# Performance work log

Hardware: AMD Instinct MI355X
Metric: run time of the kernel (lower is better)

The kernel has to match this reference:

```python
import jax, jax.numpy as jnp
import numpy as np

B, N, D, NH, L, DFF = 2, 2048, 256, 8, 4, 1024
DH = D // NH
FACTOR = 0.5 / float(np.sqrt(DH))  # == 1/sqrt(4*DH), matches q/k feature dim 4*d_head
EPS = 1e-5


def _ln(x, g, b):
    m = x.mean(-1, keepdims=True)
    v = ((x - m) ** 2).mean(-1, keepdims=True)
    return (x - m) * jax.lax.rsqrt(v + EPS) * g + b


def setup_inputs() -> dict:
    key = jax.random.key(0)
    ks = jax.random.split(key, 16)
    s = 0.05
    r = lambda i, shape: jax.random.normal(ks[i], shape, dtype=jnp.float32)
    return {
        "H": r(0, (B, N, D)),
        "V": r(1, (B, N, 3, D)),
        "D_batch": r(2, (B, N, N)),
        "rbf_feat": r(3, (L, B, 1, N, N)),
        "H_mask": jnp.ones((B, N), dtype=bool),
        "ln1_g": jnp.ones((L, D)), "ln1_b": jnp.zeros((L, D)),
        "ln2_g": jnp.ones((L, D)), "ln2_b": jnp.zeros((L, D)),
        "Wq": r(4, (L, D, 4 * D)) * s, "bq": jnp.zeros((L, 4 * D)),
        "Wk": r(5, (L, D, 4 * D)) * s, "bk": jnp.zeros((L, 4 * D)),
        "Wv": r(6, (L, D, D)) * s, "bv": jnp.zeros((L, D)),
        "Wvv": r(7, (L, D, D)) * s,
        "Wo": r(8, (L, D, D)) * s, "bo": jnp.zeros((L, D)),
        "Wvo": r(9, (L, D, D)) * s,
        "Wlv": r(10, (L, D, 2 * D)) * s,
        "W1": r(11, (L, 2 * D, DFF)) * s, "b1": jnp.zeros((L, DFF)),
        "W2": r(12, (L, DFF, 2 * D)) * s, "b2": jnp.zeros((L, 2 * D)),
    }


def _stack_forward(H, V, D_batch, rbf_feat, H_mask, ln1_g, ln1_b, ln2_g, ln2_b,
                   Wq, bq, Wk, bk, Wv, bv, Wvv, Wo, bo, Wvo, Wlv, W1, b1, W2, b2):
    b, n = H.shape[:2]
    mask = H_mask[:, None, None, :]       # [B,1,1,N] masks key columns
    base_bias = D_batch[:, None]          # [B,1,N,N]

    def step(carry, xs):
        H, V = carry
        (rbf, g1, be1, g2, be2, wq, bq_, wk, bk_, wv, bv_, wvv,
         wo, bo_, wvo, wlv, w1, b1_, w2, b2_) = xs
        # --- self-attention sublayer (pre-LN on scalar stream only) ---
        Hn = _ln(H, g1, be1)
        Hq = (Hn @ wq + bq_).reshape(b, n, NH, 4 * DH)
        Hk = (Hn @ wk + bk_).reshape(b, n, NH, 4 * DH)
        Hv = (Hn @ wv + bv_).reshape(b, n, NH, DH)
        Vv = (V @ wvv).reshape(b, n, 3, NH, DH)
        Vv = jnp.swapaxes(Vv, 2, 3).reshape(b, n, NH, 3 * DH)
        V_attn = jnp.concatenate([Hv, Vv], axis=-1)        # [B,N,H,4*DH]
        bias = jnp.where(mask, rbf + base_bias, -jnp.inf)  # [B,1,N,N]
        scores = jnp.einsum('bnhd,bmhd->bhnm', Hq, Hk) * FACTOR + bias
        attn = jax.nn.softmax(scores, axis=-1)
        res = jnp.einsum('bhnm,bmhd->bnhd', attn, V_attn)  # [B,N,H,4*DH]
        H_res = res[..., :DH].reshape(b, n, D)
        V_res = jnp.swapaxes(res[..., DH:].reshape(b, n, NH, 3, DH), 2, 3).reshape(b, n, 3, D)
        H = H + (H_res @ wo + bo_)
        V = V + V_res @ wvo
        # --- GVP FFN sublayer (pre-LN on scalar stream only) ---
        Hn = _ln(H, g2, be2)
        Vp = V @ wlv                                       # [B,N,3,2D]
        V1, V2 = Vp[..., :D], Vp[..., D:]
        scaler = jnp.concatenate([Hn, jnp.linalg.norm(V1, axis=-2)], axis=-1)
        sc = jax.nn.silu(scaler @ w1 + b1_) @ w2 + b2_
        H = H + sc[..., :D]
        V = V + sc[..., D:][..., None, :] * V2             # vector_act='none'
        return (H, V), None

    xs = (rbf_feat, ln1_g, ln1_b, ln2_g, ln2_b, Wq, bq, Wk, bk, Wv, bv, Wvv,
          Wo, bo, Wvo, Wlv, W1, b1, W2, b2)
    (H, V), _ = jax.lax.scan(step, (H, V), xs)
    return H, V


def reference(H, V, D_batch, rbf_feat, H_mask, ln1_g, ln1_b, ln2_g, ln2_b,
              Wq, bq, Wk, bk, Wv, bv, Wvv, Wo, bo, Wvo, Wlv, W1, b1, W2, b2):
    return _stack_forward(H, V, D_batch, rbf_feat, H_mask, ln1_g, ln1_b, ln2_g, ln2_b,
                          Wq, bq, Wk, bk, Wv, bv, Wvv, Wo, bo, Wvo, Wlv, W1, b1, W2, b2)
```

## Files before the change

### kernel.cpp

```cpp
#include <hip/hip_runtime.h>
#include <math.h>

static constexpr int B_  = 2;
static constexpr int N_  = 2048;
static constexpr int D_  = 256;
static constexpr int NH_ = 8;
static constexpr int L_  = 4;
static constexpr int DH_ = 32;
static constexpr int DQ_ = 128;
static constexpr float FACTOR_ = 0.08838834764831845f;
static constexpr float LOG2E_  = 1.4426950408889634f;
static constexpr float EPS_ = 1e-5f;

typedef short    short8   __attribute__((ext_vector_type(8)));
typedef unsigned short us4 __attribute__((ext_vector_type(4)));
typedef unsigned short us8 __attribute__((ext_vector_type(8)));
typedef float    f32x4    __attribute__((ext_vector_type(4)));
typedef unsigned short us;

__device__ __forceinline__ us f2b(float f) {
  unsigned u = __float_as_uint(f);
  unsigned r = u + 0x7FFF + ((u >> 16) & 1);
  return (us)(r >> 16);
}
__device__ __forceinline__ float b2f(us u) {
  return __uint_as_float(((unsigned)u) << 16);
}
__device__ __forceinline__ float e2(float x) {
  return __builtin_amdgcn_exp2f(x);
}
__device__ __forceinline__ void gl_lds16(const void* g, void* l) {
  __builtin_amdgcn_global_load_lds(
      (const __attribute__((address_space(1))) void*)g,
      (__attribute__((address_space(3))) void*)l, 16, 0, 0);
}

__global__ __launch_bounds__(256) void ln_kernel(const float* __restrict__ X,
    const float* __restrict__ g, const float* __restrict__ b,
    us* __restrict__ Y, float* __restrict__ Xcopy) {
  __shared__ float p1[4], p2[4];
  int row = blockIdx.x, tid = threadIdx.x;
  float x = X[(size_t)row * D_ + tid];
  if (Xcopy) Xcopy[(size_t)row * D_ + tid] = x;
  float a = x, c = x * x;
  #pragma unroll
  for (int o = 32; o > 0; o >>= 1) {
    a += __shfl_xor(a, o, 64);
    c += __shfl_xor(c, o, 64);
  }
  if ((tid & 63) == 0) { p1[tid >> 6] = a; p2[tid >> 6] = c; }
  __syncthreads();
  float s1 = (p1[0] + p1[1]) + (p1[2] + p1[3]);
  float s2 = (p2[0] + p2[1]) + (p2[2] + p2[3]);
  float mean = s1 * (1.0f / D_);
  float var  = s2 * (1.0f / D_) - mean * mean;
  float inv  = rsqrtf(var + EPS_);
  Y[(size_t)row * D_ + tid] = f2b((x - mean) * inv * g[tid] + b[tid]);
}

__global__ __launch_bounds__(256) void conv_copy(const float* __restrict__ X,
    float* __restrict__ Yf, us* __restrict__ Y) {
  size_t i = ((size_t)blockIdx.x * 256 + threadIdx.x) * 4;
  float4 v = *(const float4*)&X[i];
  *(float4*)&Yf[i] = v;
  us4 o = { f2b(v.x), f2b(v.y), f2b(v.z), f2b(v.w) };
  *(us4*)&Y[i] = o;
}

struct WConvDesc {
  const float* src[9];
  unsigned dst[9];
  int K[9];
  int N[9];
  int start[10];
  int lstride[9];
};
__global__ __launch_bounds__(256) void wconv_kernel(WConvDesc d, us* __restrict__ Wb) {
  __shared__ float T[64][65];
  int bid0 = blockIdx.x, tid = threadIdx.x;
  int lay = bid0 / 480;
  int bid = bid0 - lay * 480;
  int j = 0;
  #pragma unroll
  for (int q = 0; q < 8; q++) if (bid >= d.start[q + 1]) j = q + 1;
  int t = bid - d.start[j];
  int K = d.K[j], N = d.N[j];
  int tpr = N >> 6;
  int tk = t / tpr, tn = t - tk * tpr;
  const float* src = d.src[j] + (size_t)lay * d.lstride[j];
  us* dst = Wb + (size_t)lay * 1966080u + d.dst[j];
  #pragma unroll
  for (int i = 0; i < 4; i++) {
    int r = i * 16 + (tid >> 4), c = (tid & 15) * 4;
    *(float4*)&T[r][c] = *(const float4*)&src[(size_t)(tk * 64 + r) * N + tn * 64 + c];
  }
  __syncthreads();
  #pragma unroll
  for (int i = 0; i < 4; i++) {
    int n = i * 16 + (tid >> 4), k = (tid & 15) * 4;
    us4 o = { f2b(T[k][n]), f2b(T[k + 1][n]), f2b(T[k + 2][n]), f2b(T[k + 3][n]) };
    *(us4*)&dst[(size_t)(tn * 64 + n) * K + tk * 64 + k] = o;
  }
}

__global__ __launch_bounds__(256, 3) void gemm_qkv(const us* __restrict__ A,
    const us* __restrict__ Wt, const float* __restrict__ bias,
    const float* __restrict__ bias2, const float* __restrict__ bias3,
    us* __restrict__ Cb, const float* __restrict__ R,
    const float* __restrict__ Dq, us* __restrict__ BiasOut, float oscale,
    const us* __restrict__ Vbm, const us* __restrict__ WtVV,
    us* __restrict__ Vvb) {
  constexpr int BM = 128, BN = 64, K = 256, Nc = 2304;
  __shared__ us As[2][BM * 64];
  __shared__ us Bs[2][BN * 64];
  const int tid = threadIdx.x;

  if (blockIdx.y >= 54) {
    const size_t total = (size_t)B_ * N_ * N_;
    const int nb = (gridDim.y - 54) * gridDim.x;
    const int bidl = (blockIdx.y - 54) * gridDim.x + blockIdx.x;
    const size_t step = (size_t)nb * 256 * 8;
    for (size_t i = ((size_t)bidl * 256 + tid) * 8; i < total; i += step) {
      float4 r0 = *(const float4*)&R[i];
      float4 r1 = *(const float4*)&R[i + 4];
      float4 d0 = *(const float4*)&Dq[i];
      float4 d1 = *(const float4*)&Dq[i + 4];
      us8 o = { f2b((r0.x + d0.x) * LOG2E_), f2b((r0.y + d0.y) * LOG2E_),
                f2b((r0.z + d0.z) * LOG2E_), f2b((r0.w + d0.w) * LOG2E_),
                f2b((r1.x + d1.x) * LOG2E_), f2b((r1.y + d1.y) * LOG2E_),
                f2b((r1.z + d1.z) * LOG2E_), f2b((r1.w + d1.w) * LOG2E_) };
      *(us8*)&BiasOut[i] = o;
    }
    return;
  }

  const int w = tid >> 6, l = tid & 63;
  const int lx = l & 15, ly = l >> 4;
  const int wr = w >> 1, wc = w & 1;
  const int swz = (lx & 7) << 4;
  const size_t rowb = (size_t)K * 2;

  if (blockIdx.y >= 32) {
    const int q = (blockIdx.y - 32) * 36 + blockIdx.x;
    if (q >= 768) return;
    const int bn = q & 3, bm = q >> 2;
    const char* Ag = (const char*)Vbm + (size_t)(bm * 64) * K * 2;
    const char* Bg = (const char*)WtVV + (size_t)(bn * 64) * K * 2;

    #define GSTAGE2(buf, k0)                                                  \
      do {                                                                    \
        _Pragma("unroll")                                                     \
        for (int j = 0; j < 2; j++) {                                         \
          int o = j * 4096 + tid * 16;                                        \
          int r = o >> 7, cb = o & 127;                                       \
          int sc = cb ^ ((r & 7) << 4);                                       \
          gl_lds16(Ag + (size_t)r * rowb + (size_t)(k0) * 2 + sc,             \
                   &As[buf][(j * 4096 + w * 1024) >> 1]);                     \
          gl_lds16(Bg + (size_t)r * rowb + (size_t)(k0) * 2 + sc,             \
                   &Bs[buf][(j * 4096 + w * 1024) >> 1]);                     \
        }                                                                     \
      } while (0)

    f32x4 acc[2][2];
    #pragma unroll
    for (int i = 0; i < 2; i++)
      #pragma unroll
      for (int j = 0; j < 2; j++) acc[i][j] = (f32x4){0.f, 0.f, 0.f, 0.f};

    int cur = 0;
    GSTAGE2(0, 0);
    __syncthreads();
    for (int k0 = 0; k0 < K; k0 += 64) {
      if (k0 + 64 < K) GSTAGE2(cur ^ 1, k0 + 64);
      #pragma unroll
      for (int s = 0; s < 2; s++) {
        short8 af[2], bf[2];
        #pragma unroll
        for (int mt = 0; mt < 2; mt++)
          af[mt] = *(const short8*)
              &As[cur][(((wr * 32 + mt * 16 + lx) * 128) + ((s * 64 + ly * 16) ^ swz)) >> 1];
        #pragma unroll
        for (int nt = 0; nt < 2; nt++)
          bf[nt] = *(const short8*)
              &Bs[cur][(((wc * 32 + nt * 16 + lx) * 128) + ((s * 64 + ly * 16) ^ swz)) >> 1];
        __builtin_amdgcn_s_setprio(1);
        #pragma unroll
        for (int mt = 0; mt < 2; mt++)
          #pragma unroll
          for (int nt = 0; nt < 2; nt++)
            acc[mt][nt] = __builtin_amdgcn_mfma_f32_16x16x32_bf16(af[mt], bf[nt], acc[mt][nt], 0, 0, 0);
        __builtin_amdgcn_s_setprio(0);
      }
      __syncthreads();
      cur ^= 1;
    }
    #undef GSTAGE2

    #pragma unroll
    for (int nt = 0; nt < 2; nt++) {
      const int n = bn * 64 + wc * 32 + nt * 16 + lx;
      #pragma unroll
      for (int mt = 0; mt < 2; mt++) {
        #pragma unroll
        for (int r = 0; r < 4; r++) {
          const int m = bm * 64 + wr * 32 + mt * 16 + ly * 4 + r;
          Vvb[(size_t)m * 256 + n] = f2b(acc[mt][nt][r]);
        }
      }
    }
    return;
  }

  const int bn = blockIdx.x, bm = blockIdx.y;
  const char* Ag = (const char*)A + (size_t)(bm * BM) * K * 2;
  const char* Bg = (const char*)Wt + (size_t)(bn * BN) * K * 2;

  #define GSTAGE(buf, k0)                                                     \
    do {                                                                      \
      _Pragma("unroll")                                                       \
      for (int j = 0; j < 4; j++) {                                           \
        int o = j * 4096 + tid * 16;                                          \
        int r = o >> 7, cb = o & 127;                                         \
        int sc = cb ^ ((r & 7) << 4);                                         \
        gl_lds16(Ag + (size_t)r * rowb + (size_t)(k0) * 2 + sc,               \
                 &As[buf][(j * 4096 + w * 1024) >> 1]);                       \
      }                                                                       \
      _Pragma("unroll")                                                       \
      for (int j = 0; j < 2; j++) {                                           \
        int o = j * 4096 + tid * 16;                                          \
        int r = o >> 7, cb = o & 127;                                         \
        int sc = cb ^ ((r & 7) << 4);                                         \
        gl_lds16(Bg + (size_t)r * rowb + (size_t)(k0) * 2 + sc,               \
                 &Bs[buf][(j * 4096 + w * 1024) >> 1]);                       \
      }                                                                       \
    } while (0)

  f32x4 acc[4][2];
  #pragma unroll
  for (int i = 0; i < 4; i++)
    #pragma unroll
    for (int j = 0; j < 2; j++) acc[i][j] = (f32x4){0.f, 0.f, 0.f, 0.f};

  int cur = 0;
  GSTAGE(0, 0);
  __syncthreads();
  for (int k0 = 0; k0 < K; k0 += 64) {
    if (k0 + 64 < K) GSTAGE(cur ^ 1, k0 + 64);
    #pragma unroll
    for (int s = 0; s < 2; s++) {
      short8 af[4], bf[2];
      #pragma unroll
      for (int mt = 0; mt < 4; mt++)
        af[mt] = *(const short8*)
            &As[cur][(((wr * 64 + mt * 16 + lx) * 128) + ((s * 64 + ly * 16) ^ swz)) >> 1];
      #pragma unroll
      for (int nt = 0; nt < 2; nt++)
        bf[nt] = *(const short8*)
            &Bs[cur][(((wc * 32 + nt * 16 + lx) * 128) + ((s * 64 + ly * 16) ^ swz)) >> 1];
      __builtin_amdgcn_s_setprio(1);
      #pragma unroll
      for (int mt = 0; mt < 4; mt++)
        #pragma unroll
        for (int nt = 0; nt < 2; nt++)
          acc[mt][nt] = __builtin_amdgcn_mfma_f32_16x16x32_bf16(af[mt], bf[nt], acc[mt][nt], 0, 0, 0);
      __builtin_amdgcn_s_setprio(0);
    }
    __syncthreads();
    cur ^= 1;
  }
  #undef GSTAGE

  #pragma unroll
  for (int nt = 0; nt < 2; nt++) {
    const int n = bn * BN + wc * 32 + nt * 16 + lx;
    float bval, osc = oscale;
    if (n < 1024)      { bval = bias[n]; }
    else if (n < 2048) { bval = bias2[n - 1024]; osc = 1.0f; }
    else               { bval = bias3[n - 2048]; osc = 1.0f; }
    #pragma unroll
    for (int mt = 0; mt < 4; mt++) {
      #pragma unroll
      for (int r = 0; r < 4; r++) {
        const int m = bm * BM + wr * 64 + mt * 16 + ly * 4 + r;
        float v = acc[mt][nt][r] + bval;
        Cb[(size_t)m * Nc + n] = f2b(v * osc);
      }
    }
  }
}

template<int BM, int BN, int BIAS, int ACC, int SILU, int WF, int WB, int QKV, int MINW>
__global__ __launch_bounds__(256, MINW) void gemm_v2(const us* __restrict__ A,
    const us* __restrict__ Wt, const float* __restrict__ bias,
    const float* __restrict__ bias2, const float* __restrict__ bias3,
    float* __restrict__ Cf, us* __restrict__ Cb,
    int M, int K, int Nc, float oscale) {
  constexpr int NFM = BM / 32, NFN = BN / 32;
  constexpr int WSM = NFM * 16, WSN = NFN * 16;
  constexpr int NLA = BM / 32, NLB = BN / 32;
  __shared__ us As[2][BM * 64];
  __shared__ us Bs[2][BN * 64];
  const int tid = threadIdx.x;
  const int w = tid >> 6, l = tid & 63;
  const int lx = l & 15, ly = l >> 4;
  const int wr = w >> 1, wc = w & 1;
  const int bn = blockIdx.x, bm = blockIdx.y;
  const int swz = (lx & 7) << 4;
  const char* Ag = (const char*)A + (size_t)(bm * BM) * K * 2;
  const char* Bg = (const char*)Wt + (size_t)(bn * BN) * K * 2;
  const size_t rowb = (size_t)K * 2;

  #define GSTAGE(buf, k0)                                                     \
    do {                                                                      \
      _Pragma("unroll")                                                       \
      for (int j = 0; j < NLA; j++) {                                         \
        int o = j * 4096 + tid * 16;                                          \
        int r = o >> 7, cb = o & 127;                                         \
        int sc = cb ^ ((r & 7) << 4);                                         \
        gl_lds16(Ag + (size_t)r * rowb + (size_t)(k0) * 2 + sc,               \
                 &As[buf][(j * 4096 + w * 1024) >> 1]);                       \
      }                                                                       \
      _Pragma("unroll")                                                       \
      for (int j = 0; j < NLB; j++) {                                         \
        int o = j * 4096 + tid * 16;                                          \
        int r = o >> 7, cb = o & 127;                                         \
        int sc = cb ^ ((r & 7) << 4);                                         \
        gl_lds16(Bg + (size_t)r * rowb + (size_t)(k0) * 2 + sc,               \
                 &Bs[buf][(j * 4096 + w * 1024) >> 1]);                       \
      }                                                                       \
    } while (0)

  f32x4 acc[NFM][NFN];
  #pragma unroll
  for (int i = 0; i < NFM; i++)
    #pragma unroll
    for (int j = 0; j < NFN; j++) acc[i][j] = (f32x4){0.f, 0.f, 0.f, 0.f};

  int cur = 0;
  GSTAGE(0, 0);
  __syncthreads();
  for (int k0 = 0; k0 < K; k0 += 64) {
    if (k0 + 64 < K) GSTAGE(cur ^ 1, k0 + 64);
    #pragma unroll
    for (int s = 0; s < 2; s++) {
      short8 af[NFM], bf[NFN];
      #pragma unroll
      for (int mt = 0; mt < NFM; mt++)
        af[mt] = *(const short8*)
            &As[cur][(((wr * WSM + mt * 16 + lx) * 128) + ((s * 64 + ly * 16) ^ swz)) >> 1];
      #pragma unroll
      for (int nt = 0; nt < NFN; nt++)
        bf[nt] = *(const short8*)
            &Bs[cur][(((wc * WSN + nt * 16 + lx) * 128) + ((s * 64 + ly * 16) ^ swz)) >> 1];
      __builtin_amdgcn_s_setprio(1);
      #pragma unroll
      for (int mt = 0; mt < NFM; mt++)
        #pragma unroll
        for (int nt = 0; nt < NFN; nt++)
          acc[mt][nt] = __builtin_amdgcn_mfma_f32_16x16x32_bf16(af[mt], bf[nt], acc[mt][nt], 0, 0, 0);
      __builtin_amdgcn_s_setprio(0);
    }
    __syncthreads();
    cur ^= 1;
  }
  #undef GSTAGE

  #pragma unroll
  for (int nt = 0; nt < NFN; nt++) {
    const int n = bn * BN + wc * WSN + nt * 16 + lx;
    float bval = 0.f, osc = oscale;
    if (QKV) {
      if (n < 1024)      { bval = bias[n]; }
      else if (n < 2048) { bval = bias2[n - 1024]; osc = 1.0f; }
      else               { bval = bias3[n - 2048]; osc = 1.0f; }
    } else if (BIAS) {
      bval = bias[n];
    }
    #pragma unroll
    for (int mt = 0; mt < NFM; mt++) {
      #pragma unroll
      for (int r = 0; r < 4; r++) {
        const int m = bm * BM + wr * WSM + mt * 16 + ly * 4 + r;
        float v = acc[mt][nt][r] + bval;
        if (SILU) v = v / (1.f + __expf(-v));
        size_t idx = (size_t)m * Nc + n;
        if (ACC) v += Cf[idx];
        if (WF) Cf[idx] = v;
        if (WB) Cb[idx] = f2b(v * osc);
      }
    }
  }
}

__global__ __launch_bounds__(256, 3) void gemm_wo(const us* __restrict__ Hres,
    const us* __restrict__ Vres, const us* __restrict__ WtO,
    const us* __restrict__ WtVO, const float* __restrict__ bo,
    float* __restrict__ Hs, float* __restrict__ Vs, us* __restrict__ Vb) {
  constexpr int K = 256, Nc = 256;
  __shared__ us As[2][64 * 64];
  __shared__ us Bs[2][64 * 64];
  const int tid = threadIdx.x;
  const int w = tid >> 6, l = tid & 63;
  const int lx = l & 15, ly = l >> 4;
  const int wr = w >> 1, wc = w & 1;
  const int bn = blockIdx.x, bm = blockIdx.y;
  const bool isH = bm < 64;
  const int mb = isH ? bm : bm - 64;
  const int swz = (lx & 7) << 4;
  const char* Ag = (const char*)(isH ? Hres : Vres) + (size_t)(mb * 64) * K * 2;
  const char* Bg = (const char*)(isH ? WtO : WtVO) + (size_t)(bn * 64) * K * 2;
  const size_t rowb = (size_t)K * 2;

  #define GSTAGE(buf, k0)                                                     \
    do {                                                                      \
      _Pragma("unroll")                                                       \
      for (int j = 0; j < 2; j++) {                                           \
        int o = j * 4096 + tid * 16;                                          \
        int r = o >> 7, cb = o & 127;                                         \
        int sc = cb ^ ((r & 7) << 4);                                         \
        gl_lds16(Ag + (size_t)r * rowb + (size_t)(k0) * 2 + sc,               \
                 &As[buf][(j * 4096 + w * 1024) >> 1]);                       \
        gl_lds16(Bg + (size_t)r * rowb + (size_t)(k0) * 2 + sc,               \
                 &Bs[buf][(j * 4096 + w * 1024) >> 1]);                       \
      }                                                                       \
    } while (0)

  f32x4 acc[2][2];
  #pragma unroll
  for (int i = 0; i < 2; i++)
    #pragma unroll
    for (int j = 0; j < 2; j++) acc[i][j] = (f32x4){0.f, 0.f, 0.f, 0.f};

  int cur = 0;
  GSTAGE(0, 0);
  __syncthreads();
  for (int k0 = 0; k0 < K; k0 += 64) {
    if (k0 + 64 < K) GSTAGE(cur ^ 1, k0 + 64);
    #pragma unroll
    for (int s = 0; s < 2; s++) {
      short8 af[2], bf[2];
      #pragma unroll
      for (int mt = 0; mt < 2; mt++)
        af[mt] = *(const short8*)
            &As[cur][(((wr * 32 + mt * 16 + lx) * 128) + ((s * 64 + ly * 16) ^ swz)) >> 1];
      #pragma unroll
      for (int nt = 0; nt < 2; nt++)
        bf[nt] = *(const short8*)
            &Bs[cur][(((wc * 32 + nt * 16 + lx) * 128) + ((s * 64 + ly * 16) ^ swz)) >> 1];
      __builtin_amdgcn_s_setprio(1);
      #pragma unroll
      for (int mt = 0; mt < 2; mt++)
        #pragma unroll
        for (int nt = 0; nt < 2; nt++)
          acc[mt][nt] = __builtin_amdgcn_mfma_f32_16x16x32_bf16(af[mt], bf[nt], acc[mt][nt], 0, 0, 0);
      __builtin_amdgcn_s_setprio(0);
    }
    __syncthreads();
    cur ^= 1;
  }
  #undef GSTAGE

  #pragma unroll
  for (int nt = 0; nt < 2; nt++) {
    const int n = bn * 64 + wc * 32 + nt * 16 + lx;
    const float bval = isH ? bo[n] : 0.f;
    #pragma unroll
    for (int mt = 0; mt < 2; mt++) {
      #pragma unroll
      for (int r = 0; r < 4; r++) {
        const int m = mb * 64 + wr * 32 + mt * 16 + ly * 4 + r;
        size_t idx = (size_t)m * Nc + n;
        float v = acc[mt][nt][r] + bval;
        if (isH) {
          Hs[idx] += v;
        } else {
          float nv = Vs[idx] + v;
          Vs[idx] = nv;
          Vb[idx] = f2b(nv);
        }
      }
    }
  }
}

__global__ __launch_bounds__(256, 3) void gemm_w2(const us* __restrict__ A,
    const us* __restrict__ Wt, const float* __restrict__ b2,
    const float* __restrict__ Vp, float* __restrict__ Hs,
    float* __restrict__ Vs, us* __restrict__ Vb) {
  constexpr int K = 1024;
  __shared__ us As[2][64 * 64];
  __shared__ us Bs[2][64 * 64];
  const int tid = threadIdx.x;
  const int w = tid >> 6, l = tid & 63;
  const int lx = l & 15, ly = l >> 4;
  const int wr = w >> 1, wc = w & 1;
  const int bn = blockIdx.x, bm = blockIdx.y;
  const int swz = (lx & 7) << 4;
  const char* Ag = (const char*)A + (size_t)(bm * 64) * K * 2;
  const char* Bg = (const char*)Wt + (size_t)(bn * 64) * K * 2;
  const size_t rowb = (size_t)K * 2;

  #define GSTAGE(buf, k0)                                                     \
    do {                                                                      \
      _Pragma("unroll")                                                       \
      for (int j = 0; j < 2; j++) {                                           \
        int o = j * 4096 + tid * 16;                                          \
        int r = o >> 7, cb = o & 127;                                         \
        int sc = cb ^ ((r & 7) << 4);                                         \
        gl_lds16(Ag + (size_t)r * rowb + (size_t)(k0) * 2 + sc,               \
                 &As[buf][(j * 4096 + w * 1024) >> 1]);                       \
        gl_lds16(Bg + (size_t)r * rowb + (size_t)(k0) * 2 + sc,               \
                 &Bs[buf][(j * 4096 + w * 1024) >> 1]);                       \
      }                                                                      \
    } while (0)

  f32x4 acc[2][2];
  #pragma unroll
  for (int i = 0; i < 2; i++)
    #pragma unroll
    for (int j = 0; j < 2; j++) acc[i][j] = (f32x4){0.f, 0.f, 0.f, 0.f};

  int cur = 0;
  GSTAGE(0, 0);
  __syncthreads();
  for (int k0 = 0; k0 < K; k0 += 64) {
    if (k0 + 64 < K) GSTAGE(cur ^ 1, k0 + 64);
    #pragma unroll
    for (int s = 0; s < 2; s++) {
      short8 af[2], bf[2];
      #pragma unroll
      for (int mt = 0; mt < 2; mt++)
        af[mt] = *(const short8*)
            &As[cur][(((wr * 32 + mt * 16 + lx) * 128) + ((s * 64 + ly * 16) ^ swz)) >> 1];
      #pragma unroll
      for (int nt = 0; nt < 2; nt++)
        bf[nt] = *(const short8*)
            &Bs[cur][(((wc * 32 + nt * 16 + lx) * 128) + ((s * 64 + ly * 16) ^ swz)) >> 1];
      __builtin_amdgcn_s_setprio(1);
      #pragma unroll
      for (int mt = 0; mt < 2; mt++)
        #pragma unroll
        for (int nt = 0; nt < 2; nt++)
          acc[mt][nt] = __builtin_amdgcn_mfma_f32_16x16x32_bf16(af[mt], bf[nt], acc[mt][nt], 0, 0, 0);
      __builtin_amdgcn_s_setprio(0);
    }
    __syncthreads();
    cur ^= 1;
  }
  #undef GSTAGE

  const bool isH = (bn < 4);
  #pragma unroll
  for (int nt = 0; nt < 2; nt++) {
    const int n = bn * 64 + wc * 32 + nt * 16 + lx;
    const float bval = b2[n];
    #pragma unroll
    for (int mt = 0; mt < 2; mt++) {
      #pragma unroll
      for (int r = 0; r < 4; r++) {
        const int m = bm * 64 + wr * 32 + mt * 16 + ly * 4 + r;
        float v = acc[mt][nt][r] + bval;
        if (isH) {
          Hs[(size_t)m * D_ + n] += v;
        } else {
          const int j = n - 256;
          #pragma unroll
          for (int c = 0; c < 3; c++) {
            size_t vi = ((size_t)m * 3 + c) * D_ + j;
            float nv = Vs[vi] + v * Vp[((size_t)m * 3 + c) * 512 + 256 + j];
            Vs[vi] = nv;
            Vb[vi] = f2b(nv);
          }
        }
      }
    }
  }
}

__global__ __launch_bounds__(256) void pack_vattn_t(const us* __restrict__ QKVb,
    const us* __restrict__ Vv, us* __restrict__ Vt) {
  __shared__ us T[64][136];
  const int bid = blockIdx.x;
  const int nt = bid & 31, hh = (bid >> 5) & 7, b = bid >> 8;
  const int n0 = nt * 64;
  const int tid = threadIdx.x;
  {
    const int nn = tid >> 2, part = tid & 3;
    const size_t row = (size_t)(b * N_ + n0 + nn);
    const us* src = (part == 0) ? (QKVb + row * 2304 + 2048 + hh * DH_)
                                : (Vv + (row * 3 + (part - 1)) * D_ + hh * DH_);
    #pragma unroll
    for (int jj = 0; jj < 32; jj += 8)
      *(us8*)&T[nn][part * 32 + jj] = *(const us8*)(src + jj);
  }
  __syncthreads();
  const int d = tid >> 1, half = tid & 1;
  size_t ob = ((size_t)(b * NH_ + hh) * DQ_ + d) * (size_t)N_ + n0 + half * 32;
  #pragma unroll
  for (int i = 0; i < 32; i += 8) {
    us8 o;
    #pragma unroll
    for (int e = 0; e < 8; e++) o[e] = T[half * 32 + i + e][d];
    *(us8*)&Vt[ob + i] = o;
  }
}

__global__ __launch_bounds__(256, 3) void attn_mfma(
    const us* __restrict__ QKVb,
    const us* __restrict__ Vtb,
    const us* __restrict__ bias,
    us* __restrict__ Hres,
    us* __restrict__ Vres) {
  __shared__ us Kt[8192];
  __shared__ us Vt[8192];
  __shared__ us Plds[4][16][72];
  const int bid = blockIdx.x;
  const int h  = bid & 7;
  const int g  = bid >> 3;
  const int b  = g >> 5;
  const int qt = g & 31;
  const int tid = threadIdx.x;
  const int w  = tid >> 6;
  const int l  = tid & 63;
  const int lx = l & 15;
  const int ly = l >> 4;
  const int qrow = qt * 64 + w * 16 + lx;
  const int swz = (lx & 7) << 4;

  short8 qf[4];
  {
    const us* qp = QKVb + (size_t)(b * N_ + qrow) * 2304 + h * DQ_ + ly * 8;
    #pragma unroll
    for (int s = 0; s < 4; s++) qf[s] = *(const short8*)(qp + s * 32);
  }
  const char* kg = (const char*)QKVb + (size_t)b * N_ * 4608 + 2048 + h * 256;
  const char* vg = (const char*)(Vtb + ((size_t)(b * NH_ + h) * DQ_) * (size_t)N_);
  const us* bbase = bias + ((size_t)b * N_ + qrow) * N_;

  us8 kreg[4], vreg[4];
  #define LOADKV(m0)                                                          \
    do {                                                                      \
      _Pragma("unroll")                                                       \
      for (int j = 0; j < 4; j++) {                                           \
        int o = j * 4096 + tid * 16;                                          \
        int rk = o >> 8, ck = o & 255;                                        \
        kreg[j] = *(const us8*)(kg + (size_t)((m0) + rk) * 4608 +             \
                                (ck ^ ((rk & 7) << 4)));                      \
        int rv = o >> 7, cv = o & 127;                                        \
        vreg[j] = *(const us8*)(vg + (size_t)rv * (N_ * 2) +                  \
                                (size_t)(m0) * 2 + (cv ^ ((rv & 7) << 4)));   \
      }                                                                       \
    } while (0)
  #define WRITEKV()                                                           \
    do {                                                                      \
      _Pragma("unroll")                                                       \
      for (int j = 0; j < 4; j++) {                                           \
        *(us8*)&Kt[j * 2048 + tid * 8] = kreg[j];                             \
        *(us8*)&Vt[j * 2048 + tid * 8] = vreg[j];                             \
      }                                                                       \
    } while (0)

  float m_run = -3.0e38f, l_run = 0.f;
  f32x4 oacc[8];
  #pragma unroll
  for (int i = 0; i < 8; i++) oacc[i] = (f32x4){0.f, 0.f, 0.f, 0.f};

  LOADKV(0);
  WRITEKV();
  LOADKV(64);
  us4 bb[4];
  #pragma unroll
  for (int t = 0; t < 4; t++) bb[t] = *(const us4*)(bbase + t * 16 + ly * 4);
  __syncthreads();

  for (int mc0 = 0; mc0 < N_; mc0 += 64) {
    us4 bbn[4];
    if (mc0 + 64 < N_) {
      #pragma unroll
      for (int t = 0; t < 4; t++)
        bbn[t] = *(const us4*)(bbase + mc0 + 64 + t * 16 + ly * 4);
    }
    f32x4 sacc[4];
    #pragma unroll
    for (int t = 0; t < 4; t++) sacc[t] = (f32x4){0.f, 0.f, 0.f, 0.f};
    __builtin_amdgcn_s_setprio(1);
    #pragma unroll
    for (int t = 0; t < 4; t++) {
      #pragma unroll
      for (int s = 0; s < 4; s++) {
        const short8 kf = *(const short8*)
            &Kt[((t * 16 + lx) * 256 + ((s * 64 + ly * 16) ^ swz)) >> 1];
        sacc[t] = __builtin_amdgcn_mfma_f32_16x16x32_bf16(kf, qf[s], sacc[t], 0, 0, 0);
      }
    }
    __builtin_amdgcn_s_setprio(0);
    float pvv[16];
    #pragma unroll
    for (int t = 0; t < 4; t++) {
      pvv[t*4+0] = sacc[t][0] + b2f(bb[t][0]);
      pvv[t*4+1] = sacc[t][1] + b2f(bb[t][1]);
      pvv[t*4+2] = sacc[t][2] + b2f(bb[t][2]);
      pvv[t*4+3] = sacc[t][3] + b2f(bb[t][3]);
    }
    float a8[8], a4[4];
    #pragma unroll
    for (int i = 0; i < 8; i++) a8[i] = fmaxf(pvv[i], pvv[i + 8]);
    #pragma unroll
    for (int i = 0; i < 4; i++) a4[i] = fmaxf(a8[i], a8[i + 4]);
    float mloc = fmaxf(fmaxf(a4[0], a4[1]), fmaxf(a4[2], a4[3]));
    if (!__all(mloc - m_run <= 11.54f)) {
      mloc = fmaxf(mloc, __shfl_xor(mloc, 16, 64));
      mloc = fmaxf(mloc, __shfl_xor(mloc, 32, 64));
      float m_new = fmaxf(m_run, mloc);
      float scale = e2(m_run - m_new);
      l_run *= scale;
      #pragma unroll
      for (int i = 0; i < 8; i++) {
        oacc[i][0] *= scale; oacc[i][1] *= scale;
        oacc[i][2] *= scale; oacc[i][3] *= scale;
      }
      m_run = m_new;
    }
    float s8[8], s4[4];
    #pragma unroll
    for (int i = 0; i < 16; i++) pvv[i] = e2(pvv[i] - m_run);
    #pragma unroll
    for (int i = 0; i < 8; i++) s8[i] = pvv[i] + pvv[i + 8];
    #pragma unroll
    for (int i = 0; i < 4; i++) s4[i] = s8[i] + s8[i + 4];
    l_run += (s4[0] + s4[1]) + (s4[2] + s4[3]);
    #pragma unroll
    for (int t = 0; t < 4; t++) {
      us4 pk = { f2b(pvv[t*4+0]), f2b(pvv[t*4+1]), f2b(pvv[t*4+2]), f2b(pvv[t*4+3]) };
      *(us4*)&Plds[w][lx][t * 16 + ly * 4] = pk;
    }
    short8 pf0 = *(const short8*)&Plds[w][lx][ly * 8];
    short8 pf1 = *(const short8*)&Plds[w][lx][32 + ly * 8];
    __builtin_amdgcn_s_setprio(1);
    #pragma unroll
    for (int dt = 0; dt < 8; dt++) {
      const int rb = (dt * 16 + lx) * 128;
      const short8 vf0 = *(const short8*)&Vt[(rb + ((ly * 16) ^ swz)) >> 1];
      const short8 vf1 = *(const short8*)&Vt[(rb + ((64 + ly * 16) ^ swz)) >> 1];
      oacc[dt] = __builtin_amdgcn_mfma_f32_16x16x32_bf16(vf0, pf0, oacc[dt], 0, 0, 0);
      oacc[dt] = __builtin_amdgcn_mfma_f32_16x16x32_bf16(vf1, pf1, oacc[dt], 0, 0, 0);
    }
    __builtin_amdgcn_s_setprio(0);
    __syncthreads();
    if (mc0 + 64 < N_) {
      WRITEKV();
      if (mc0 + 128 < N_) LOADKV(mc0 + 128);
      #pragma unroll
      for (int t = 0; t < 4; t++) bb[t] = bbn[t];
      __syncthreads();
    }
  }
  #undef LOADKV
  #undef WRITEKV
  l_run += __shfl_xor(l_run, 16, 64);
  l_run += __shfl_xor(l_run, 32, 64);
  float inv = 1.0f / l_run;
  const size_t row = (size_t)(b * N_ + qrow);
  #pragma unroll
  for (int dt = 0; dt < 8; dt++) {
    const int d0 = dt * 16 + ly * 4;
    us4 pk = { f2b(oacc[dt][0] * inv), f2b(oacc[dt][1] * inv),
               f2b(oacc[dt][2] * inv), f2b(oacc[dt][3] * inv) };
    if (d0 < 32) {
      *(us4*)&Hres[row * D_ + h * DH_ + d0] = pk;
    } else {
      const int c = (d0 - DH_) >> 5, dd = (d0 - DH_) & 31;
      *(us4*)&Vres[(row * 3 + c) * D_ + h * DH_ + dd] = pk;
    }
  }
}

__global__ __launch_bounds__(256) void ln2scaler(const float* __restrict__ H,
    const float* __restrict__ g, const float* __restrict__ b,
    const float* __restrict__ Vp, us* __restrict__ scal) {
  __shared__ float p1[4], p2[4];
  size_t row = blockIdx.x;
  int j = threadIdx.x;
  float x = H[row * D_ + j];
  float a = x, c = x * x;
  #pragma unroll
  for (int o = 32; o > 0; o >>= 1) {
    a += __shfl_xor(a, o, 64);
    c += __shfl_xor(c, o, 64);
  }
  if ((j & 63) == 0) { p1[j >> 6] = a; p2[j >> 6] = c; }
  __syncthreads();
  float s1 = (p1[0] + p1[1]) + (p1[2] + p1[3]);
  float s2 = (p2[0] + p2[1]) + (p2[2] + p2[3]);
  float mean = s1 * (1.0f / D_);
  float var  = s2 * (1.0f / D_) - mean * mean;
  float inv  = rsqrtf(var + EPS_);
  scal[row * 512 + j] = f2b((x - mean) * inv * g[j] + b[j]);
  float va = Vp[(row * 3 + 0) * 512 + j];
  float c1 = Vp[(row * 3 + 1) * 512 + j];
  float c2 = Vp[(row * 3 + 2) * 512 + j];
  scal[row * 512 + D_ + j] = f2b(sqrtf(va * va + c1 * c1 + c2 * c2));
}

extern "C" void kernel_launch(void* const* d_in, const int* in_sizes, int n_in,
                              void* d_out, int out_size, void* d_ws, size_t ws_size,
                              hipStream_t stream) {
  const float* H_in = (const float*)d_in[0];
  const float* V_in = (const float*)d_in[1];
  const float* Db   = (const float*)d_in[2];
  const float* rbf  = (const float*)d_in[3];
  const float* ln1g = (const float*)d_in[5];
  const float* ln1b = (const float*)d_in[6];
  const float* ln2g = (const float*)d_in[7];
  const float* ln2b = (const float*)d_in[8];
  const float* Wq  = (const float*)d_in[9];
  const float* bq  = (const float*)d_in[10];
  const float* Wk  = (const float*)d_in[11];
  const float* bk  = (const float*)d_in[12];
  const float* Wv  = (const float*)d_in[13];
  const float* bv  = (const float*)d_in[14];
  const float* Wvv = (const float*)d_in[15];
  const float* Wo  = (const float*)d_in[16];
  const float* bo  = (const float*)d_in[17];
  const float* Wvo = (const float*)d_in[18];
  const float* Wlv = (const float*)d_in[19];
  const float* W1  = (const float*)d_in[20];
  const float* b1  = (const float*)d_in[21];
  const float* W2  = (const float*)d_in[22];
  const float* b2  = (const float*)d_in[23];

  const size_t HN = (size_t)B_ * N_ * D_;
  const size_t VN = HN * 3;
  float* Hs = (float*)d_out;
  float* Vs = (float*)d_out + HN;
  float* ws = (float*)d_ws;
  us*    bias_b = (us*)ws;
  us*    Vb     = (us*)(ws + 5177344);
  us*    Hnb    = (us*)(ws + 6750208);
  us*    QKVb   = (us*)(ws + 7274496);
  us*    Vtb    = (us*)(ws + 11993088);
  us*    Vvb    = (us*)(ws + 14090240);
  us*    Hres_b = (us*)(ws + 6750208);
  us*    Vres_b = (us*)(ws + 14090240);
  float* Vp     = ws + 7274496;
  us*    scal_b = (us*)(ws + 13565952);
  us*    midb   = (us*)(ws + 15014528);
  us*    Wb4    = (us*)(ws + 17111680);

  conv_copy<<<3072, 256, 0, stream>>>(V_in, Vs, Vb);

  const int ROWS  = B_ * N_;
  static const int wKs[9] = {256,256,256,256,256,256,256,512,1024};
  static const int wNs[9] = {1024,1024,256,256,256,256,512,1024,512};
  static const unsigned wOff[9] = {0,262144,524288,589824,655360,720896,786432,917504,1441792};
  static const int wStart[10] = {0,64,128,144,160,176,192,224,352,480};
  static const int wLstr[9] = {262144,262144,65536,65536,65536,65536,131072,524288,524288};

  {
    WConvDesc dsc;
    const float* srcs[9] = {Wq, Wk, Wv, Wvv, Wo, Wvo, Wlv, W1, W2};
    for (int j = 0; j < 9; j++) {
      dsc.src[j] = srcs[j]; dsc.dst[j] = wOff[j];
      dsc.K[j] = wKs[j]; dsc.N[j] = wNs[j]; dsc.start[j] = wStart[j];
      dsc.lstride[j] = wLstr[j];
    }
    dsc.start[9] = wStart[9];
    wconv_kernel<<<480 * L_, 256, 0, stream>>>(dsc, Wb4);
  }
  ln_kernel<<<ROWS, 256, 0, stream>>>(H_in, ln1g, ln1b, Hnb, Hs);

  for (int l = 0; l < L_; ++l) {
    us* Wb = Wb4 + (size_t)l * 1966080u;

    gemm_qkv<<<dim3(36, 66), 256, 0, stream>>>(
        Hnb, Wb + wOff[0], bq + l * 1024, bk + l * 1024, bv + l * 256,
        QKVb, rbf + (size_t)l * B_ * N_ * N_, Db, bias_b, FACTOR_ * LOG2E_,
        Vb, Wb + wOff[3], Vvb);
    pack_vattn_t<<<512, 256, 0, stream>>>(QKVb, Vvb, Vtb);
    attn_mfma<<<512, 256, 0, stream>>>(QKVb, Vtb, bias_b, Hres_b, Vres_b);
    gemm_wo<<<dim3(4, 256), 256, 0, stream>>>(
        Hres_b, Vres_b, Wb + wOff[4], Wb + wOff[5], bo + l * 256, Hs, Vs, Vb);
    gemm_v2<128,64,0,0,0,1,0,0,3><<<dim3(8, 96), 256, 0, stream>>>(
        Vb, Wb + wOff[6], nullptr, nullptr, nullptr, Vp, nullptr, 12288, 256, 512, 1.f);
    ln2scaler<<<ROWS, 256, 0, stream>>>(Hs, ln2g + l * D_, ln2b + l * D_, Vp, scal_b);
    gemm_v2<128,64,1,0,1,0,1,0,3><<<dim3(16, 32), 256, 0, stream>>>(
        scal_b, Wb + wOff[7], b1 + l * 1024, nullptr, nullptr, nullptr, midb, 4096, 512, 1024, 1.f);
    gemm_w2<<<dim3(8, 64), 256, 0, stream>>>(
        midb, Wb + wOff[8], b2 + l * 512, Vp, Hs, Vs, Vb);
    if (l < 3)
      ln_kernel<<<ROWS, 256, 0, stream>>>(Hs, ln1g + (l + 1) * D_,
                                          ln1b + (l + 1) * D_, Hnb, nullptr);
  }
}
```

Before: 745.9 us.

## Split attention KV range in two with a separate combine kernel

The attention kernel now splits the key/value sequence into two halves, launching twice as many blocks. Each writes unnormalized fp32 partial outputs plus its running max and sum to workspace. A new combine kernel merges the two partials with log-sum-exp weights and writes the bf16 Hres/Vres outputs. The aim is better occupancy on a 256-CU device, where 512 blocks leave CUs underused. The cost is extra fp32 partial traffic and one more kernel launch per layer.

```diff
diff --git a/kernel.cpp b/kernel.cpp
--- a/kernel.cpp
+++ b/kernel.cpp
@@ -609,16 +609,19 @@
     const us* __restrict__ QKVb,
     const us* __restrict__ Vtb,
     const us* __restrict__ bias,
-    us* __restrict__ Hres,
-    us* __restrict__ Vres) {
+    float* __restrict__ Opart,
+    float* __restrict__ Ml) {
   __shared__ us Kt[8192];
   __shared__ us Vt[8192];
   __shared__ us Plds[4][16][72];
   const int bid = blockIdx.x;
   const int h  = bid & 7;
   const int g  = bid >> 3;
-  const int b  = g >> 5;
   const int qt = g & 31;
+  const int bs = g >> 5;
+  const int b  = bs & 1;
+  const int sp = bs >> 1;
+  const int kv0 = sp * 1024;
   const int tid = threadIdx.x;
   const int w  = tid >> 6;
   const int l  = tid & 63;
@@ -665,17 +668,18 @@
   #pragma unroll
   for (int i = 0; i < 8; i++) oacc[i] = (f32x4){0.f, 0.f, 0.f, 0.f};
 
-  LOADKV(0);
+  LOADKV(kv0);
   WRITEKV();
-  LOADKV(64);
+  LOADKV(kv0 + 64);
   us4 bb[4];
   #pragma unroll
-  for (int t = 0; t < 4; t++) bb[t] = *(const us4*)(bbase + t * 16 + ly * 4);
+  for (int t = 0; t < 4; t++) bb[t] = *(const us4*)(bbase + kv0 + t * 16 + ly * 4);
   __syncthreads();
 
-  for (int mc0 = 0; mc0 < N_; mc0 += 64) {
+  const int kvend = kv0 + 1024;
+  for (int mc0 = kv0; mc0 < kvend; mc0 += 64) {
     us4 bbn[4];
-    if (mc0 + 64 < N_) {
+    if (mc0 + 64 < kvend) {
       #pragma unroll
       for (int t = 0; t < 4; t++)
         bbn[t] = *(const us4*)(bbase + mc0 + 64 + t * 16 + ly * 4);
@@ -747,9 +751,9 @@
     }
     __builtin_amdgcn_s_setprio(0);
     __syncthreads();
-    if (mc0 + 64 < N_) {
+    if (mc0 + 64 < kvend) {
       WRITEKV();
-      if (mc0 + 128 < N_) LOADKV(mc0 + 128);
+      if (mc0 + 128 < kvend) LOADKV(mc0 + 128);
       #pragma unroll
       for (int t = 0; t < 4; t++) bb[t] = bbn[t];
       __syncthreads();
@@ -759,19 +763,43 @@
   #undef WRITEKV
   l_run += __shfl_xor(l_run, 16, 64);
   l_run += __shfl_xor(l_run, 32, 64);
-  float inv = 1.0f / l_run;
-  const size_t row = (size_t)(b * N_ + qrow);
-  #pragma unroll
-  for (int dt = 0; dt < 8; dt++) {
-    const int d0 = dt * 16 + ly * 4;
-    us4 pk = { f2b(oacc[dt][0] * inv), f2b(oacc[dt][1] * inv),
-               f2b(oacc[dt][2] * inv), f2b(oacc[dt][3] * inv) };
-    if (d0 < 32) {
-      *(us4*)&Hres[row * D_ + h * DH_ + d0] = pk;
-    } else {
-      const int c = (d0 - DH_) >> 5, dd = (d0 - DH_) & 31;
-      *(us4*)&Vres[(row * 3 + c) * D_ + h * DH_ + dd] = pk;
-    }
+  const size_t grow = (size_t)(b * N_ + qrow);
+  const size_t rh = ((size_t)sp * 4096 + grow) * 8 + h;
+  float* op = Opart + rh * 128;
+  #pragma unroll
+  for (int dt = 0; dt < 8; dt++)
+    *(f32x4*)&op[dt * 16 + ly * 4] = oacc[dt];
+  if (ly == 0) {
+    Ml[rh * 2 + 0] = m_run;
+    Ml[rh * 2 + 1] = l_run;
+  }
+}
+
+__global__ __launch_bounds__(256) void attn_combine(
+    const float* __restrict__ Opart, const float* __restrict__ Ml,
+    us* __restrict__ Hres, us* __restrict__ Vres) {
+  const size_t grow = blockIdx.x;
+  const int tid = threadIdx.x;
+  const int h = tid >> 5;
+  const int d = (tid & 31) * 4;
+  const size_t rh0 = grow * 8 + h;
+  const size_t rh1 = ((size_t)4096 + grow) * 8 + h;
+  const float m0 = Ml[rh0 * 2], l0 = Ml[rh0 * 2 + 1];
+  const float m1 = Ml[rh1 * 2], l1 = Ml[rh1 * 2 + 1];
+  const float M  = fmaxf(m0, m1);
+  const float w0 = e2(m0 - M), w1 = e2(m1 - M);
+  const float inv = 1.0f / (l0 * w0 + l1 * w1);
+  f32x4 o0 = *(const f32x4*)&Opart[rh0 * 128 + d];
+  f32x4 o1 = *(const f32x4*)&Opart[rh1 * 128 + d];
+  us4 pk;
+  #pragma unroll
+  for (int e = 0; e < 4; e++)
+    pk[e] = f2b((o0[e] * w0 + o1[e] * w1) * inv);
+  if (d < 32) {
+    *(us4*)&Hres[grow * D_ + h * DH_ + d] = pk;
+  } else {
+    const int c = (d - DH_) >> 5, dd = (d - DH_) & 31;
+    *(us4*)&Vres[(grow * 3 + c) * D_ + h * DH_ + dd] = pk;
   }
 }
 
@@ -846,6 +874,8 @@
   us*    scal_b = (us*)(ws + 13565952);
   us*    midb   = (us*)(ws + 15014528);
   us*    Wb4    = (us*)(ws + 17111680);
+  float* Opart  = ws + 21043840;
+  float* Mlp    = ws + 29432448;
 
   conv_copy<<<3072, 256, 0, stream>>>(V_in, Vs, Vb);
 
@@ -877,7 +907,8 @@
         QKVb, rbf + (size_t)l * B_ * N_ * N_, Db, bias_b, FACTOR_ * LOG2E_,
         Vb, Wb + wOff[3], Vvb);
     pack_vattn_t<<<512, 256, 0, stream>>>(QKVb, Vvb, Vtb);
-    attn_mfma<<<512, 256, 0, stream>>>(QKVb, Vtb, bias_b, Hres_b, Vres_b);
+    attn_mfma<<<1024, 256, 0, stream>>>(QKVb, Vtb, bias_b, Opart, Mlp);
+    attn_combine<<<ROWS, 256, 0, stream>>>(Opart, Mlp, Hres_b, Vres_b);
     gemm_wo<<<dim3(4, 256), 256, 0, stream>>>(
         Hres_b, Vres_b, Wb + wOff[4], Wb + wOff[5], bo + l * 256, Hs, Vs, Vb);
     gemm_v2<128,64,0,0,0,1,0,0,3><<<dim3(8, 96), 256, 0, stream>>>(
```

New measurement: 830.6 us. 11.4% more time.
